# Optimization experiments

Measured on AMD Instinct MI355X. Metric: run time of the kernel, lower is better.

The kernel has to match this reference:

```python
import jax, jax.numpy as jnp
import numpy as np

NH = 8          # num_heads
NEG = -1e30     # mask_logits fill value


def setup_inputs() -> dict:
    key = jax.random.key(0)
    k1, k2, k3, k4 = jax.random.split(key, 4)
    B, D, T = 4, 1024, 2048
    x = jax.random.normal(k1, (B, D, T), dtype=jnp.float32)
    mask = jax.random.randint(k2, (B, T), 0, 2).astype(jnp.float32)
    # xavier-uniform-ish linear weights, torch layout [out, in]
    lim = float(np.sqrt(6.0 / (D + D)))
    Wq = jax.random.uniform(k3, (D, D), dtype=jnp.float32, minval=-lim, maxval=lim)
    Wo = jax.random.uniform(k4, (D, D), dtype=jnp.float32, minval=-lim, maxval=lim)
    return {"x": x, "mask": mask, "Wq": Wq, "Wo": Wo}


def reference(x, mask, Wq, Wo):
    # x: [B, D, T] channels-first; mask: [B, T] in {0,1} float
    B, D, T = x.shape
    dk = D // NH
    scale = 1.0 / jnp.sqrt(jnp.asarray(dk, x.dtype))
    xt = jnp.transpose(x, (0, 2, 1))                 # [B, T, D]
    # NOTE: original source uses Wqs for Q, K and V (source bug, reproduced)
    q = xt @ Wq.T                                    # [B, T, D]
    qh = q.reshape(B, T, NH, dk).transpose(0, 2, 1, 3)  # [B, H, T, dk]
    scores = scale * jnp.einsum('bhqd,bhkd->bhqk', qh, qh)  # [B, H, T, T]
    cmask = mask[:, None, None, :]                   # column mask [B,1,1,T]
    rmask = mask[:, None, :, None]                   # row mask    [B,1,T,1]
    logits = (scores * cmask + (1.0 - cmask) * NEG) * rmask
    attn = jax.nn.softmax(logits, axis=-1)
    ctx = jnp.einsum('bhqk,bhkd->bhqd', attn, qh)    # [B, H, T, dk]
    ctx = ctx.transpose(0, 2, 1, 3).reshape(B, T, D)
    out = ctx @ Wo.T                                 # [B, T, D]
    return jnp.transpose(out, (0, 2, 1))             # [B, D, T]
```

## Files before the change

### kernel.cpp

```cpp
#include <hip/hip_runtime.h>

#define TT 2048
#define DD 1024
#define NHH 8
#define DKK 128
#define SCALE2 0.1275174724f

typedef __attribute__((ext_vector_type(8)))  short short8;
typedef __attribute__((ext_vector_type(4)))  short short4v;
typedef __attribute__((ext_vector_type(4)))  float float4v;
typedef __attribute__((ext_vector_type(16))) float float16v;
typedef __attribute__((ext_vector_type(4)))  int   int4v;

__device__ __forceinline__ short f2bf(float f) {
  union { float f; unsigned u; } v; v.f = f;
  unsigned r = v.u + 0x7FFFu + ((v.u >> 16) & 1u);
  return (short)(r >> 16);
}
__device__ __forceinline__ unsigned cvtpk(float lo, float hi) {
  unsigned r;
  asm("v_cvt_pk_bf16_f32 %0, %1, %2" : "=v"(r) : "v"(lo), "v"(hi));
  return r;
}
__device__ __forceinline__ float xhalf_add(float x) {
  float y;
  asm("v_mov_b32 %0, %1" : "=v"(y) : "v"(x));
  asm("v_permlane32_swap_b32 %0, %1" : "+v"(x), "+v"(y));
  return x + y;
}
__device__ __forceinline__ int s4(int row) {
  return (row & 7) ^ (((row >> 3) & 3) << 2);
}

__global__ __launch_bounds__(256) void k_xt(const float* __restrict__ x,
                                            short* __restrict__ xt) {
  __shared__ float tile[32][33];
  int b = blockIdx.z, d0 = blockIdx.y << 5, t0 = blockIdx.x << 5;
  int tx = threadIdx.x & 31, ty = threadIdx.x >> 5;
  const float* xp = x + ((size_t)b * DD + d0) * TT + t0;
#pragma unroll
  for (int yy = 0; yy < 32; yy += 8)
    tile[ty + yy][tx] = xp[(size_t)(ty + yy) * TT + tx];
  __syncthreads();
  short* op = xt + ((size_t)b * TT + t0) * DD + d0;
#pragma unroll
  for (int yy = 0; yy < 32; yy += 8)
    op[(size_t)(ty + yy) * DD + tx] = f2bf(tile[tx][ty + yy]);
}

__global__ void k_cast(const float* __restrict__ w, short* __restrict__ o, int n4) {
  int i = blockIdx.x * 256 + threadIdx.x;
  if (i < n4) {
    float4v v = ((const float4v*)w)[i];
    short4v s;
#pragma unroll
    for (int j = 0; j < 4; ++j) s[j] = f2bf(v[j]);
    ((short4v*)o)[i] = s;
  }
}

__global__ __launch_bounds__(256) void k_qt(const short* __restrict__ qb,
                                            short* __restrict__ qhT) {
  __shared__ short tile[64][65];
  int b = blockIdx.z, n0 = blockIdx.y << 6, t0 = blockIdx.x << 6;
  int tx = threadIdx.x & 63, ty = threadIdx.x >> 6;
  const short* ip = qb + ((size_t)(b * TT + t0)) * DD + n0;
#pragma unroll
  for (int yy = 0; yy < 64; yy += 4)
    tile[ty + yy][tx] = ip[(size_t)(ty + yy) * DD + tx];
  __syncthreads();
  short* op = qhT + ((size_t)(b * DD + n0)) * TT + t0;
#pragma unroll
  for (int yy = 0; yy < 64; yy += 4)
    op[(size_t)(ty + yy) * TT + tx] = tile[tx][ty + yy];
}

template <int EPI>
__global__ __launch_bounds__(256) void k_gemm(const short* __restrict__ A,
                                              const short* __restrict__ Bt,
                                              void* __restrict__ Cout) {
  __shared__ short As[128][72];
  __shared__ short Bs[128][72];
  const int K = 1024;
  int tm = blockIdx.x * 128, tn = blockIdx.y * 128;
  int tid = threadIdx.x, lane = tid & 63, w = tid >> 6;
  int wm = (w >> 1) * 64, wn = (w & 1) * 64;
  int g = lane >> 4;

  float4v acc[4][4];
#pragma unroll
  for (int mt = 0; mt < 4; ++mt)
#pragma unroll
    for (int nt = 0; nt < 4; ++nt) acc[mt][nt] = (float4v){0.f, 0.f, 0.f, 0.f};

  for (int k0 = 0; k0 < K; k0 += 64) {
    __syncthreads();
#pragma unroll
    for (int c = 0; c < 4; ++c) {
      int chunk = tid + 256 * c;
      int row = chunk >> 3, col8 = chunk & 7;
      int4v va = *(const int4v*)(A + (size_t)(tm + row) * K + k0 + col8 * 8);
      *(int4v*)(&As[row][col8 * 8]) = va;
      int4v vb = *(const int4v*)(Bt + (size_t)(tn + row) * K + k0 + col8 * 8);
      *(int4v*)(&Bs[row][col8 * 8]) = vb;
    }
    __syncthreads();
#pragma unroll
    for (int k4 = 0; k4 < 2; ++k4) {
      int kk = k4 * 32 + g * 8;
      short8 af[4], bfr[4];
#pragma unroll
      for (int mt = 0; mt < 4; ++mt)
        af[mt] = *(const short8*)(&As[wm + mt * 16 + (lane & 15)][kk]);
#pragma unroll
      for (int nt = 0; nt < 4; ++nt)
        bfr[nt] = *(const short8*)(&Bs[wn + nt * 16 + (lane & 15)][kk]);
#pragma unroll
      for (int mt = 0; mt < 4; ++mt)
#pragma unroll
        for (int nt = 0; nt < 4; ++nt)
          acc[mt][nt] = __builtin_amdgcn_mfma_f32_16x16x32_bf16(af[mt], bfr[nt],
                                                                acc[mt][nt], 0, 0, 0);
    }
  }

#pragma unroll
  for (int mt = 0; mt < 4; ++mt)
#pragma unroll
    for (int nt = 0; nt < 4; ++nt)
#pragma unroll
      for (int r = 0; r < 4; ++r) {
        int m = tm + wm + mt * 16 + g * 4 + r;
        int n = tn + wn + nt * 16 + (lane & 15);
        float v = acc[mt][nt][r];
        if (EPI == 0) {
          ((short*)Cout)[(size_t)m * 1024 + n] = f2bf(v);
        } else {
          int b = n >> 11, t = n & 2047;
          ((float*)Cout)[((size_t)b * 1024 + m) * 2048 + t] = v;
        }
      }
}

__global__ __launch_bounds__(256, 2) void k_attn(const short* __restrict__ q,
                                                 const short* __restrict__ qhT,
                                                 const float* __restrict__ mask,
                                                 short* __restrict__ ctx) {
  __shared__ __align__(16) short Ks[2][64 * 128];
  __shared__ __align__(16) short Vt[2][128 * 64];
  __shared__ __align__(16) short Kx[2][64 * 16];

  int qt = blockIdx.x, bh = blockIdx.y;
  int b = bh >> 3, h = bh & 7;
  int tid = threadIdx.x, lane = tid & 63, w = tid >> 6;
  int ql32 = lane & 31, hi = lane >> 5;
  int csw = s4(ql32);
  int vsw = ql32 & 7;
  short negbig = f2bf(-1e30f);

  int qrow = qt * 128 + w * 32 + ql32;
  const short* qp = q + ((size_t)(b * TT + qrow)) * DD + h * DKK;
  short8 qf[8];
#pragma unroll
  for (int kc8 = 0; kc8 < 8; ++kc8)
    qf[kc8] = *(const short8*)(qp + kc8 * 16 + hi * 8);
  float rm = mask[(size_t)b * TT + qrow];

  float qs = SCALE2 * rm;
#pragma unroll
  for (int kc8 = 0; kc8 < 8; ++kc8) {
    union { short8 s; unsigned u[4]; } a;
    a.s = qf[kc8];
#pragma unroll
    for (int j = 0; j < 4; ++j) {
      union { unsigned u; float f; } lo, hh;
      lo.u = a.u[j] << 16;
      hh.u = a.u[j] & 0xFFFF0000u;
      a.u[j] = cvtpk(lo.f * qs, hh.f * qs);
    }
    qf[kc8] = a.s;
  }
  short8 bext = (short8)0;
  if (hi == 0) bext[0] = (rm != 0.f) ? (short)0x3F80 : (short)0;

  int oc = tid & 15, r2 = tid >> 4;
  const short* kbase_g = q + ((size_t)b * TT) * DD + h * DKK + oc * 8;
  const short* vbase_g = qhT + ((size_t)(b * DD + h * DKK)) * TT;
  int vd[4], vko[4], vwoff[4];
#pragma unroll
  for (int p = 0; p < 4; ++p) {
    int idx = p * 256 + tid;
    vd[p] = idx >> 3;
    vko[p] = idx & 7;
    vwoff[p] = vd[p] * 64 + ((vko[p] ^ (vd[p] & 7)) * 8);
  }
  int kwoff[2][2];
#pragma unroll
  for (int ps = 0; ps < 2; ++ps) {
    int ra = 2 * r2 + 32 * ps, rb = ra + 1;
    kwoff[ps][0] = ra * 128 + ((oc ^ s4(ra)) * 8);
    kwoff[ps][1] = rb * 128 + ((oc ^ s4(rb)) * 8);
  }

  short8 va[2], vb[2], vv[4];
#pragma unroll
  for (int ps = 0; ps < 2; ++ps) {
    const short* kp = kbase_g + (size_t)(2 * r2 + 32 * ps) * DD;
    va[ps] = *(const short8*)(kp);
    vb[ps] = *(const short8*)(kp + DD);
  }
#pragma unroll
  for (int p = 0; p < 4; ++p)
    vv[p] = *(const short8*)(vbase_g + (size_t)vd[p] * TT + vko[p] * 8);
  float mreg = mask[(size_t)b * TT + lane];

#pragma unroll
  for (int ps = 0; ps < 2; ++ps) {
    *(short8*)(Ks[0] + kwoff[ps][0]) = va[ps];
    *(short8*)(Ks[0] + kwoff[ps][1]) = vb[ps];
  }
#pragma unroll
  for (int p = 0; p < 4; ++p)
    *(short8*)(Vt[0] + vwoff[p]) = vv[p];
  if (tid < 128) {
    short8 z = (short8)0;
    if (tid < 64) z[0] = (mreg != 0.f) ? (short)0 : negbig;
    *(short8*)(&Kx[0][0] + tid * 16) = z;
    *(short8*)(&Kx[0][0] + tid * 16 + 8) = (short8)0;
  }

  float l_run = 0.f;
  float16v o[4];
#pragma unroll
  for (int nt = 0; nt < 4; ++nt)
#pragma unroll
    for (int r = 0; r < 16; ++r) o[nt][r] = 0.f;

  for (int kt = 0; kt < 32; ++kt) {
    int cur = kt & 1;
    const short* ksb = Ks[cur];
    const short* vtb = Vt[cur];
    const short* kxb = Kx[cur];
    short* ksn = Ks[cur ^ 1];
    short* vtn = Vt[cur ^ 1];
    short* kxn = Kx[cur ^ 1];

    __syncthreads();

    if (kt < 31) {
      int kb0n = (kt + 1) * 64;
      const short* kpn = kbase_g + (size_t)kb0n * DD;
#pragma unroll
      for (int ps = 0; ps < 2; ++ps) {
        const short* kp = kpn + (size_t)(2 * r2 + 32 * ps) * DD;
        va[ps] = *(const short8*)(kp);
        vb[ps] = *(const short8*)(kp + DD);
      }
#pragma unroll
      for (int p = 0; p < 4; ++p)
        vv[p] = *(const short8*)(vbase_g + (size_t)vd[p] * TT + kb0n + vko[p] * 8);
      mreg = mask[(size_t)b * TT + kb0n + lane];
    }

    float16v st0, st1;
#pragma unroll
    for (int r = 0; r < 16; ++r) { st0[r] = 0.f; st1[r] = 0.f; }
    __builtin_amdgcn_s_setprio(1);
    {
      short8 ax0 = *(const short8*)(kxb + ql32 * 16 + hi * 8);
      short8 ax1 = *(const short8*)(kxb + (32 + ql32) * 16 + hi * 8);
      st0 = __builtin_amdgcn_mfma_f32_32x32x16_bf16(ax0, bext, st0, 0, 0, 0);
      st1 = __builtin_amdgcn_mfma_f32_32x32x16_bf16(ax1, bext, st1, 0, 0, 0);
    }
#pragma unroll
    for (int kc8 = 0; kc8 < 8; ++kc8) {
      int csk = ((kc8 * 2 + hi) ^ csw) * 8;
      short8 kf0 = *(const short8*)(ksb + ql32 * 128 + csk);
      short8 kf1 = *(const short8*)(ksb + (32 + ql32) * 128 + csk);
      st0 = __builtin_amdgcn_mfma_f32_32x32x16_bf16(kf0, qf[kc8], st0, 0, 0, 0);
      st1 = __builtin_amdgcn_mfma_f32_32x32x16_bf16(kf1, qf[kc8], st1, 0, 0, 0);
    }
    __builtin_amdgcn_s_setprio(0);

    float tsum = 0.f;
#pragma unroll
    for (int r = 0; r < 16; ++r) {
      float p0 = __builtin_amdgcn_exp2f(st0[r]);
      float p1 = __builtin_amdgcn_exp2f(st1[r]);
      st0[r] = p0; st1[r] = p1;
      tsum += p0 + p1;
    }
    l_run += xhalf_add(tsum);

    short8 pa[4];
#pragma unroll
    for (int kc = 0; kc < 4; ++kc) {
      int a0 = 2 * (kc & 1);
      unsigned x0, x1, y0, y1;
      if (kc < 2) {
        x0 = cvtpk(st0[4 * a0 + 0], st0[4 * a0 + 1]);
        x1 = cvtpk(st0[4 * a0 + 2], st0[4 * a0 + 3]);
        y0 = cvtpk(st0[4 * a0 + 4], st0[4 * a0 + 5]);
        y1 = cvtpk(st0[4 * a0 + 6], st0[4 * a0 + 7]);
      } else {
        x0 = cvtpk(st1[4 * a0 + 0], st1[4 * a0 + 1]);
        x1 = cvtpk(st1[4 * a0 + 2], st1[4 * a0 + 3]);
        y0 = cvtpk(st1[4 * a0 + 4], st1[4 * a0 + 5]);
        y1 = cvtpk(st1[4 * a0 + 6], st1[4 * a0 + 7]);
      }
      asm("v_permlane32_swap_b32 %0, %1" : "+v"(x0), "+v"(y0));
      asm("v_permlane32_swap_b32 %0, %1" : "+v"(x1), "+v"(y1));
      union { unsigned u[4]; short8 s8; } pu;
      pu.u[0] = x0; pu.u[1] = x1; pu.u[2] = y0; pu.u[3] = y1;
      pa[kc] = pu.s8;
    }

    __builtin_amdgcn_s_setprio(1);
#pragma unroll
    for (int nt = 0; nt < 4; ++nt) {
      int row = nt * 32 + ql32;
#pragma unroll
      for (int kc = 0; kc < 4; ++kc) {
        short8 vf = *(const short8*)(vtb + row * 64 + (((kc * 2 + hi) ^ vsw) * 8));
        o[nt] = __builtin_amdgcn_mfma_f32_32x32x16_bf16(vf, pa[kc], o[nt], 0, 0, 0);
      }
    }
    __builtin_amdgcn_s_setprio(0);

    if (kt < 31) {
#pragma unroll
      for (int ps = 0; ps < 2; ++ps) {
        *(short8*)(ksn + kwoff[ps][0]) = va[ps];
        *(short8*)(ksn + kwoff[ps][1]) = vb[ps];
      }
#pragma unroll
      for (int p = 0; p < 4; ++p)
        *(short8*)(vtn + vwoff[p]) = vv[p];
      if (tid < 64) {
        unsigned word = (mreg != 0.f) ? 0u : (unsigned)(unsigned short)negbig;
        *(unsigned*)(kxn + tid * 16) = word;
      }
    }
  }

  float il = 1.0f / l_run;
  short* cp = ctx + ((size_t)(b * TT + qrow)) * DD + h * DKK;
#pragma unroll
  for (int nt = 0; nt < 4; ++nt)
#pragma unroll
    for (int a = 0; a < 4; ++a) {
      short4v sv;
#pragma unroll
      for (int j = 0; j < 4; ++j) sv[j] = f2bf(o[nt][4 * a + j] * il);
      *(short4v*)(cp + nt * 32 + 8 * a + 4 * hi) = sv;
    }
}

extern "C" void kernel_launch(void* const* d_in, const int* in_sizes, int n_in,
                              void* d_out, int out_size, void* d_ws, size_t ws_size,
                              hipStream_t stream) {
  const float* x    = (const float*)d_in[0];
  const float* mask = (const float*)d_in[1];
  const float* Wq   = (const float*)d_in[2];
  const float* Wo   = (const float*)d_in[3];
  char* ws = (char*)d_ws;
  short* xt  = (short*)(ws);
  short* wqb = (short*)(ws + (size_t)16 * 1024 * 1024);
  short* wob = (short*)(ws + (size_t)18 * 1024 * 1024);
  short* qb  = (short*)(ws + (size_t)20 * 1024 * 1024);
  short* ctx = (short*)(ws + (size_t)36 * 1024 * 1024);
  short* qhT = xt;

  k_xt<<<dim3(64, 32, 4), 256, 0, stream>>>(x, xt);
  k_cast<<<1024, 256, 0, stream>>>(Wq, wqb, 262144);
  k_cast<<<1024, 256, 0, stream>>>(Wo, wob, 262144);
  k_gemm<0><<<dim3(64, 8), 256, 0, stream>>>(xt, wqb, qb);
  k_qt<<<dim3(32, 16, 4), 256, 0, stream>>>(qb, qhT);
  k_attn<<<dim3(16, 32), 256, 0, stream>>>(qb, qhT, mask, ctx);
  k_gemm<1><<<dim3(8, 64), 256, 0, stream>>>(wob, ctx, d_out);
}
```

Measured before the change: 152.6 us.

## Use direct global-to-LDS loads with swizzled layout in GEMM and attention

Replaces register-staged global loads followed by LDS stores with global_load_lds direct transfers in both the projection GEMM and the attention kernel. Global source addresses are XOR-swizzled so the linear per-wave LDS destination matches the swizzled read pattern, and the padded GEMM tiles become unpadded and swizzled. This is meant to free VGPRs and remove the separate LDS store instructions. Correctness now depends on the swizzle mapping and on LDS visibility at the existing barriers, since the direct loads complete asynchronously.

```diff
diff --git a/kernel.cpp b/kernel.cpp
--- a/kernel.cpp
+++ b/kernel.cpp
@@ -30,6 +30,11 @@
 }
 __device__ __forceinline__ int s4(int row) {
   return (row & 7) ^ (((row >> 3) & 3) << 2);
+}
+__device__ __forceinline__ void gl2lds(const void* g, void* l) {
+  __builtin_amdgcn_global_load_lds(
+      (const __attribute__((address_space(1))) void*)g,
+      (__attribute__((address_space(3))) void*)l, 16, 0, 0);
 }
 
 __global__ __launch_bounds__(256) void k_xt(const float* __restrict__ x,
@@ -79,13 +84,22 @@
 __global__ __launch_bounds__(256) void k_gemm(const short* __restrict__ A,
                                               const short* __restrict__ Bt,
                                               void* __restrict__ Cout) {
-  __shared__ short As[128][72];
-  __shared__ short Bs[128][72];
+  __shared__ __align__(16) short As[128 * 64];
+  __shared__ __align__(16) short Bs[128 * 64];
   const int K = 1024;
   int tm = blockIdx.x * 128, tn = blockIdx.y * 128;
   int tid = threadIdx.x, lane = tid & 63, w = tid >> 6;
   int wm = (w >> 1) * 64, wn = (w & 1) * 64;
-  int g = lane >> 4;
+  int ql = lane & 15, g = lane >> 4;
+
+  int srow[4], scol[4];
+#pragma unroll
+  for (int c = 0; c < 4; ++c) {
+    int cg = w * 4 + c;
+    int r = cg * 8 + (lane >> 3);
+    srow[c] = r;
+    scol[c] = ((lane & 7) ^ (r & 7)) * 8;
+  }
 
   float4v acc[4][4];
 #pragma unroll
@@ -97,24 +111,24 @@
     __syncthreads();
 #pragma unroll
     for (int c = 0; c < 4; ++c) {
-      int chunk = tid + 256 * c;
-      int row = chunk >> 3, col8 = chunk & 7;
-      int4v va = *(const int4v*)(A + (size_t)(tm + row) * K + k0 + col8 * 8);
-      *(int4v*)(&As[row][col8 * 8]) = va;
-      int4v vb = *(const int4v*)(Bt + (size_t)(tn + row) * K + k0 + col8 * 8);
-      *(int4v*)(&Bs[row][col8 * 8]) = vb;
+      int cg = w * 4 + c;
+      gl2lds(A + (size_t)(tm + srow[c]) * K + k0 + scol[c], As + cg * 512);
+      gl2lds(Bt + (size_t)(tn + srow[c]) * K + k0 + scol[c], Bs + cg * 512);
     }
     __syncthreads();
 #pragma unroll
     for (int k4 = 0; k4 < 2; ++k4) {
-      int kk = k4 * 32 + g * 8;
       short8 af[4], bfr[4];
 #pragma unroll
-      for (int mt = 0; mt < 4; ++mt)
-        af[mt] = *(const short8*)(&As[wm + mt * 16 + (lane & 15)][kk]);
-#pragma unroll
-      for (int nt = 0; nt < 4; ++nt)
-        bfr[nt] = *(const short8*)(&Bs[wn + nt * 16 + (lane & 15)][kk]);
+      for (int mt = 0; mt < 4; ++mt) {
+        int row = wm + mt * 16 + ql;
+        af[mt] = *(const short8*)(As + row * 64 + (((k4 * 4 + g) ^ (ql & 7)) * 8));
+      }
+#pragma unroll
+      for (int nt = 0; nt < 4; ++nt) {
+        int row = wn + nt * 16 + ql;
+        bfr[nt] = *(const short8*)(Bs + row * 64 + (((k4 * 4 + g) ^ (ql & 7)) * 8));
+      }
 #pragma unroll
       for (int mt = 0; mt < 4; ++mt)
 #pragma unroll
@@ -131,7 +145,7 @@
 #pragma unroll
       for (int r = 0; r < 4; ++r) {
         int m = tm + wm + mt * 16 + g * 4 + r;
-        int n = tn + wn + nt * 16 + (lane & 15);
+        int n = tn + wn + nt * 16 + ql;
         float v = acc[mt][nt][r];
         if (EPI == 0) {
           ((short*)Cout)[(size_t)m * 1024 + n] = f2bf(v);
@@ -183,45 +197,27 @@
   short8 bext = (short8)0;
   if (hi == 0) bext[0] = (rm != 0.f) ? (short)0x3F80 : (short)0;
 
-  int oc = tid & 15, r2 = tid >> 4;
-  const short* kbase_g = q + ((size_t)b * TT) * DD + h * DKK + oc * 8;
+  int krow[4], kcol[4], vrow[4], vcol[4];
+#pragma unroll
+  for (int c = 0; c < 4; ++c) {
+    int cg = w * 4 + c;
+    int kr = cg * 4 + (lane >> 4);
+    krow[c] = kr;
+    kcol[c] = (((lane & 15) ^ s4(kr)) * 8);
+    int vr = cg * 8 + (lane >> 3);
+    vrow[c] = vr;
+    vcol[c] = (((lane & 7) ^ (vr & 7)) * 8);
+  }
+  const short* kbase_g = q + ((size_t)b * TT) * DD + h * DKK;
   const short* vbase_g = qhT + ((size_t)(b * DD + h * DKK)) * TT;
-  int vd[4], vko[4], vwoff[4];
-#pragma unroll
-  for (int p = 0; p < 4; ++p) {
-    int idx = p * 256 + tid;
-    vd[p] = idx >> 3;
-    vko[p] = idx & 7;
-    vwoff[p] = vd[p] * 64 + ((vko[p] ^ (vd[p] & 7)) * 8);
-  }
-  int kwoff[2][2];
-#pragma unroll
-  for (int ps = 0; ps < 2; ++ps) {
-    int ra = 2 * r2 + 32 * ps, rb = ra + 1;
-    kwoff[ps][0] = ra * 128 + ((oc ^ s4(ra)) * 8);
-    kwoff[ps][1] = rb * 128 + ((oc ^ s4(rb)) * 8);
-  }
-
-  short8 va[2], vb[2], vv[4];
-#pragma unroll
-  for (int ps = 0; ps < 2; ++ps) {
-    const short* kp = kbase_g + (size_t)(2 * r2 + 32 * ps) * DD;
-    va[ps] = *(const short8*)(kp);
-    vb[ps] = *(const short8*)(kp + DD);
-  }
-#pragma unroll
-  for (int p = 0; p < 4; ++p)
-    vv[p] = *(const short8*)(vbase_g + (size_t)vd[p] * TT + vko[p] * 8);
+
   float mreg = mask[(size_t)b * TT + lane];
-
-#pragma unroll
-  for (int ps = 0; ps < 2; ++ps) {
-    *(short8*)(Ks[0] + kwoff[ps][0]) = va[ps];
-    *(short8*)(Ks[0] + kwoff[ps][1]) = vb[ps];
-  }
-#pragma unroll
-  for (int p = 0; p < 4; ++p)
-    *(short8*)(Vt[0] + vwoff[p]) = vv[p];
+#pragma unroll
+  for (int c = 0; c < 4; ++c) {
+    int cg = w * 4 + c;
+    gl2lds(kbase_g + (size_t)krow[c] * DD + kcol[c], Ks[0] + cg * 512);
+    gl2lds(vbase_g + (size_t)vrow[c] * TT + vcol[c], Vt[0] + cg * 512);
+  }
   if (tid < 128) {
     short8 z = (short8)0;
     if (tid < 64) z[0] = (mreg != 0.f) ? (short)0 : negbig;
@@ -249,16 +245,12 @@
 
     if (kt < 31) {
       int kb0n = (kt + 1) * 64;
-      const short* kpn = kbase_g + (size_t)kb0n * DD;
-#pragma unroll
-      for (int ps = 0; ps < 2; ++ps) {
-        const short* kp = kpn + (size_t)(2 * r2 + 32 * ps) * DD;
-        va[ps] = *(const short8*)(kp);
-        vb[ps] = *(const short8*)(kp + DD);
-      }
-#pragma unroll
-      for (int p = 0; p < 4; ++p)
-        vv[p] = *(const short8*)(vbase_g + (size_t)vd[p] * TT + kb0n + vko[p] * 8);
+#pragma unroll
+      for (int c = 0; c < 4; ++c) {
+        int cg = w * 4 + c;
+        gl2lds(kbase_g + (size_t)(kb0n + krow[c]) * DD + kcol[c], ksn + cg * 512);
+        gl2lds(vbase_g + (size_t)vrow[c] * TT + kb0n + vcol[c], vtn + cg * 512);
+      }
       mreg = mask[(size_t)b * TT + kb0n + lane];
     }
 
@@ -327,19 +319,9 @@
     }
     __builtin_amdgcn_s_setprio(0);
 
-    if (kt < 31) {
-#pragma unroll
-      for (int ps = 0; ps < 2; ++ps) {
-        *(short8*)(ksn + kwoff[ps][0]) = va[ps];
-        *(short8*)(ksn + kwoff[ps][1]) = vb[ps];
-      }
-#pragma unroll
-      for (int p = 0; p < 4; ++p)
-        *(short8*)(vtn + vwoff[p]) = vv[p];
-      if (tid < 64) {
-        unsigned word = (mreg != 0.f) ? 0u : (unsigned)(unsigned short)negbig;
-        *(unsigned*)(kxn + tid * 16) = word;
-      }
+    if (kt < 31 && tid < 64) {
+      unsigned word = (mreg != 0.f) ? 0u : (unsigned)(unsigned short)negbig;
+      *(unsigned*)(kxn + tid * 16) = word;
     }
   }
 
```

Measured after the change: 156.1 us. 2.3% more time.
